# Performance work log

Measured on AMD Instinct MI355X. Metric: run time of the kernel, lower is better.

## Reference

```python
import jax, jax.numpy as jnp
import numpy as np

H = 512      # hidden_size
Z = 128      # z_dim
E = 512      # embedding_dim
D = 2 * H + Z  # GRU hidden / decoder state dim = 1152
V = 32000    # output_size
BS = 256
N = 128      # encoder nodes per source


def setup_inputs() -> dict:
    key = jax.random.key(0)
    ks = jax.random.split(key, 24)
    s = 0.05
    inp = {
        "prev_y": jax.random.normal(ks[0], (BS, E), jnp.float32),
        "prev_h": jax.random.normal(ks[1], (BS, D), jnp.float32),
        "equ_enc": jax.random.normal(ks[2], (BS, N, H), jnp.float32),
        "sns_enc": jax.random.normal(ks[3], (BS, N, H), jnp.float32),
        "z_sample": jax.random.normal(ks[4], (BS, Z), jnp.float32),
        "equ_mask": jax.random.randint(ks[5], (BS, N), 0, 2) > 0,
        "sns_mask": jax.random.randint(ks[6], (BS, N), 0, 2) > 0,
        # Attention (equ): W1: HxH, W2: HxD, vt: 1xH (torch Linear weight = [out,in])
        "W1e": jax.random.normal(ks[7], (H, H), jnp.float32) * s,
        "W2e": jax.random.normal(ks[8], (H, D), jnp.float32) * s,
        "vte": jax.random.normal(ks[9], (1, H), jnp.float32) * s,
        "W1s": jax.random.normal(ks[10], (H, H), jnp.float32) * s,
        "W2s": jax.random.normal(ks[11], (H, D), jnp.float32) * s,
        "vts": jax.random.normal(ks[12], (1, H), jnp.float32) * s,
        "plan_W": jax.random.normal(ks[13], (2, D), jnp.float32) * s,
        "plan_b": jax.random.normal(ks[14], (2,), jnp.float32) * s,
        "Wc": jax.random.normal(ks[15], (H, E + H), jnp.float32) * s,
        "bc": jax.random.normal(ks[16], (H,), jnp.float32) * s,
        # GRU: input H -> hidden D
        "w_ih": jax.random.normal(ks[17], (3 * D, H), jnp.float32) * s,
        "w_hh": jax.random.normal(ks[18], (3 * D, D), jnp.float32) * s,
        "b_ih": jax.random.normal(ks[19], (3 * D,), jnp.float32) * s,
        "b_hh": jax.random.normal(ks[20], (3 * D,), jnp.float32) * s,
        "Wout": jax.random.normal(ks[21], (V, D), jnp.float32) * s,
        "bout": jax.random.normal(ks[22], (V,), jnp.float32) * s,
    }
    return inp


def _attn(h, enc, mask, W1, W2, vt):
    # enc: (b,n,H), h: (b,D)
    et = jnp.einsum('bnh,kh->bnk', enc, W1)          # (b,n,H)
    dt = (h @ W2.T)[:, None, :]                       # (b,1,H)
    u = jnp.einsum('bnh,h->bn', jnp.tanh(et + dt), vt[0])
    u = jnp.where(mask, -jnp.inf, u)
    return jax.nn.softmax(u, axis=-1)                 # (b,n)


def reference(prev_y, prev_h, equ_enc, sns_enc, z_sample, equ_mask, sns_mask,
              W1e, W2e, vte, W1s, W2s, vts, plan_W, plan_b, Wc, bc,
              w_ih, w_hh, b_ih, b_hh, Wout, bout):
    aw_e = _attn(prev_h, equ_enc, equ_mask, W1e, W2e, vte)
    ctx_e = jnp.einsum('bn,bnh->bh', aw_e, equ_enc)
    aw_s = _attn(prev_h, sns_enc, sns_mask, W1s, W2s, vts)
    ctx_s = jnp.einsum('bn,bnh->bh', aw_s, sns_enc)
    plan = jax.nn.softmax(prev_h @ plan_W.T + plan_b, axis=-1)  # (b,2)
    combine = jnp.stack([ctx_e, ctx_s], axis=1)                  # (b,2,H)
    context = jnp.einsum('bk,bkh->bh', plan, combine)
    y_ctx = jnp.concatenate([prev_y, context], axis=-1)          # (b,E+H)
    x = y_ctx @ Wc.T + bc                                        # (b,H)
    # single-step GRU (torch gate order: r, z, n)
    gx = x @ w_ih.T + b_ih                                       # (b,3D)
    gh = prev_h @ w_hh.T + b_hh
    Dh = prev_h.shape[-1]
    gx_r, gx_z, gx_n = gx[:, :Dh], gx[:, Dh:2*Dh], gx[:, 2*Dh:]
    gh_r, gh_z, gh_n = gh[:, :Dh], gh[:, Dh:2*Dh], gh[:, 2*Dh:]
    r = jax.nn.sigmoid(gx_r + gh_r)
    zg = jax.nn.sigmoid(gx_z + gh_z)
    n = jnp.tanh(gx_n + r * gh_n)
    h_new = (1.0 - zg) * n + zg * prev_h                          # (b,D)
    dec_output = (h_new @ Wout.T + bout)[:, None, :]              # (b,1,V)
    dec_hidden = h_new[None]                                      # (1,b,D)
    return dec_output, dec_hidden, plan
```

## Files before the change

### kernel.cpp

```cpp
#include <hip/hip_runtime.h>
#include <stdint.h>
#include <math.h>

#define BS_  256
#define NSEQ 128
#define HH   512
#define DD   1152
#define VV   32000
#define BN_  (BS_*NSEQ)

typedef float  f32x4  __attribute__((ext_vector_type(4)));
typedef __bf16 bf16x8 __attribute__((ext_vector_type(8)));

__device__ __forceinline__ f32x4 mfma16(bf16x8 a, bf16x8 b, f32x4 c) {
    return __builtin_amdgcn_mfma_f32_16x16x32_bf16(a, b, c, 0, 0, 0);
}

__device__ __forceinline__ bf16x8 pack8(f32x4 a, f32x4 b) {
    bf16x8 v;
    v[0] = (__bf16)a[0]; v[1] = (__bf16)a[1]; v[2] = (__bf16)a[2]; v[3] = (__bf16)a[3];
    v[4] = (__bf16)b[0]; v[5] = (__bf16)b[1]; v[6] = (__bf16)b[2]; v[7] = (__bf16)b[3];
    return v;
}

__device__ __forceinline__ float tanh_fast(float x) {
    float e = __expf(2.f * x);
    return 1.f - __fdividef(2.f, e + 1.f);
}

__global__ __launch_bounds__(256) void k_tile128(
    const float* __restrict__ A, const float* __restrict__ B,
    const float* __restrict__ bias, float* __restrict__ C,
    int K, int ldc)
{
    const int rb = blockIdx.x * 128;
    const int cb = blockIdx.y * 128;
    const int t = threadIdx.x;
    const int w = t >> 6, wr = w >> 1, wc = w & 1;
    const int lane = t & 63, g = lane >> 4, r = lane & 15;
    const int s_row = t >> 1, s_h = t & 1;

    __shared__ bf16x8 sm[2][2][512];

    const float* Ap = A + (size_t)(rb + s_row) * K + s_h * 16;
    const float* Bp = B + (size_t)(cb + s_row) * K + s_h * 16;

    const int kg0 = 2 * s_h, kg1 = 2 * s_h + 1;
    const int swz0 = kg0 * 128 + ((s_row & 112) | ((s_row ^ (kg0 << 2)) & 15));
    const int swz1 = kg1 * 128 + ((s_row & 112) | ((s_row ^ (kg1 << 2)) & 15));

    int ai[4], bi[4];
    #pragma unroll
    for (int i = 0; i < 4; ++i) {
        ai[i] = g * 128 + wr * 64 + i * 16 + ((r ^ (g << 2)) & 15);
        bi[i] = g * 128 + wc * 64 + i * 16 + ((r ^ (g << 2)) & 15);
    }

    const int KS = K >> 5;
    f32x4 pa0 = ((const f32x4*)Ap)[0], pa1 = ((const f32x4*)Ap)[1],
          pa2 = ((const f32x4*)Ap)[2], pa3 = ((const f32x4*)Ap)[3];
    f32x4 pb0 = ((const f32x4*)Bp)[0], pb1 = ((const f32x4*)Bp)[1],
          pb2 = ((const f32x4*)Bp)[2], pb3 = ((const f32x4*)Bp)[3];

    f32x4 acc[4][4];
    #pragma unroll
    for (int i = 0; i < 4; ++i)
        #pragma unroll
        for (int j = 0; j < 4; ++j) acc[i][j] = (f32x4){0.f, 0.f, 0.f, 0.f};

    for (int kb = 0; kb < KS; ++kb) {
        const int buf = kb & 1;
        sm[buf][0][swz0] = pack8(pa0, pa1);
        sm[buf][0][swz1] = pack8(pa2, pa3);
        sm[buf][1][swz0] = pack8(pb0, pb1);
        sm[buf][1][swz1] = pack8(pb2, pb3);
        __syncthreads();
        if (kb + 1 < KS) {
            const float* a2 = Ap + (kb + 1) * 32;
            const float* b2 = Bp + (kb + 1) * 32;
            pa0 = ((const f32x4*)a2)[0]; pa1 = ((const f32x4*)a2)[1];
            pa2 = ((const f32x4*)a2)[2]; pa3 = ((const f32x4*)a2)[3];
            pb0 = ((const f32x4*)b2)[0]; pb1 = ((const f32x4*)b2)[1];
            pb2 = ((const f32x4*)b2)[2]; pb3 = ((const f32x4*)b2)[3];
        }
        bf16x8 af[4], bfr[4];
        #pragma unroll
        for (int i = 0; i < 4; ++i) af[i]  = sm[buf][0][ai[i]];
        #pragma unroll
        for (int j = 0; j < 4; ++j) bfr[j] = sm[buf][1][bi[j]];
        #pragma unroll
        for (int i = 0; i < 4; ++i)
            #pragma unroll
            for (int j = 0; j < 4; ++j)
                acc[i][j] = mfma16(af[i], bfr[j], acc[i][j]);
    }

    #pragma unroll
    for (int j = 0; j < 4; ++j) {
        const int col = cb + wc * 64 + j * 16 + r;
        const float bv = bias ? bias[col] : 0.f;
        #pragma unroll
        for (int i = 0; i < 4; ++i) {
            #pragma unroll
            for (int q = 0; q < 4; ++q) {
                const int row = rb + wr * 64 + i * 16 + g * 4 + q;
                C[(size_t)row * ldc + col] = acc[i][j][q] + bv;
            }
        }
    }
}

__global__ __launch_bounds__(256) void k_prevh(
    const float* __restrict__ prev_h, const float* __restrict__ W2e,
    const float* __restrict__ W2s, const float* __restrict__ w_hh,
    const float* __restrict__ b_hh,
    float* __restrict__ dt_e, float* __restrict__ dt_s, float* __restrict__ gh)
{
    const int cb = blockIdx.x * 64;
    const int rb = blockIdx.y * 64;
    const int t  = threadIdx.x;
    const int w = t >> 6, lane = t & 63, g = lane >> 4, r = lane & 15;
    const int s_row = t >> 2, s_kc = t & 3;
    const int K = DD;

    __shared__ bf16x8 sm[2][2][256];

    const float* Ap = prev_h + (size_t)(rb + s_row) * K + s_kc * 8;
    const float* Bp;
    {
        int brow = cb + s_row;
        if (cb < 512)        Bp = W2e + (size_t)brow * K;
        else if (cb < 1024)  Bp = W2s + (size_t)(brow - 512) * K;
        else                 Bp = w_hh + (size_t)(brow - 1024) * K;
        Bp += s_kc * 8;
    }

    const int KS = K >> 5;
    f32x4 pa0 = *(const f32x4*)Ap, pa1 = *(const f32x4*)(Ap + 4);
    f32x4 pb0 = *(const f32x4*)Bp, pb1 = *(const f32x4*)(Bp + 4);

    f32x4 acc[4] = {{0,0,0,0},{0,0,0,0},{0,0,0,0},{0,0,0,0}};

    for (int kb = 0; kb < KS; ++kb) {
        sm[kb & 1][0][s_kc * 64 + s_row] = pack8(pa0, pa1);
        sm[kb & 1][1][s_kc * 64 + s_row] = pack8(pb0, pb1);
        __syncthreads();
        if (kb + 1 < KS) {
            const float* a2 = Ap + (kb + 1) * 32;
            const float* b2 = Bp + (kb + 1) * 32;
            pa0 = *(const f32x4*)a2; pa1 = *(const f32x4*)(a2 + 4);
            pb0 = *(const f32x4*)b2; pb1 = *(const f32x4*)(b2 + 4);
        }
        bf16x8 af = sm[kb & 1][0][g * 64 + w * 16 + r];
        #pragma unroll
        for (int j = 0; j < 4; ++j) {
            bf16x8 bf = sm[kb & 1][1][g * 64 + j * 16 + r];
            acc[j] = mfma16(af, bf, acc[j]);
        }
    }

    #pragma unroll
    for (int j = 0; j < 4; ++j) {
        int col = cb + j * 16 + r;
        #pragma unroll
        for (int q = 0; q < 4; ++q) {
            int row = rb + w * 16 + g * 4 + q;
            float v = acc[j][q];
            if (cb < 512)       dt_e[(size_t)row * 512 + col] = v;
            else if (cb < 1024) dt_s[(size_t)row * 512 + (col - 512)] = v;
            else {
                int c0 = col - 1024;
                gh[(size_t)row * 3456 + c0] = v + b_hh[c0];
            }
        }
    }
}

__global__ __launch_bounds__(256) void k_attn(
    const float* __restrict__ enc_e, const float* __restrict__ enc_s,
    const float* __restrict__ W1e, const float* __restrict__ W1s,
    const float* __restrict__ vte, const float* __restrict__ vts,
    const float* __restrict__ dt_e, const float* __restrict__ dt_s,
    float* __restrict__ u)
{
    const int b = blockIdx.x;
    const int e = blockIdx.y;
    const float* enc = e ? enc_s : enc_e;
    const float* W1  = e ? W1s  : W1e;
    const float* vt  = e ? vts  : vte;
    const float* dt  = e ? dt_s : dt_e;

    __shared__ bf16x8 sm[2][2][512];
    __shared__ float uacc[128];

    const int t = threadIdx.x;
    const int w = t >> 6, wr = w >> 1, wc = w & 1;
    const int lane = t & 63, g = lane >> 4, r = lane & 15;
    const int s_row = t >> 1, s_h = t & 1;

    if (t < 128) uacc[t] = 0.f;

    const int kg0 = 2 * s_h, kg1 = 2 * s_h + 1;
    const int swz0 = kg0 * 128 + ((s_row & 112) | ((s_row ^ (kg0 << 2)) & 15));
    const int swz1 = kg1 * 128 + ((s_row & 112) | ((s_row ^ (kg1 << 2)) & 15));

    int ai[4], bi[4];
    #pragma unroll
    for (int i = 0; i < 4; ++i) {
        ai[i] = g * 128 + wr * 64 + i * 16 + ((r ^ (g << 2)) & 15);
        bi[i] = g * 128 + wc * 64 + i * 16 + ((r ^ (g << 2)) & 15);
    }

    const float* Abase = enc + (size_t)(b * 128 + s_row) * 512 + s_h * 16;

    f32x4 pa0, pa1, pa2, pa3, pb0, pb1, pb2, pb3;
    {
        const float* ap = Abase;
        const float* bp = W1 + (size_t)s_row * 512 + s_h * 16;
        pa0 = ((const f32x4*)ap)[0]; pa1 = ((const f32x4*)ap)[1];
        pa2 = ((const f32x4*)ap)[2]; pa3 = ((const f32x4*)ap)[3];
        pb0 = ((const f32x4*)bp)[0]; pb1 = ((const f32x4*)bp)[1];
        pb2 = ((const f32x4*)bp)[2]; pb3 = ((const f32x4*)bp)[3];
    }

    for (int nc = 0; nc < 4; ++nc) {
        f32x4 acc[4][4];
        #pragma unroll
        for (int i = 0; i < 4; ++i)
            #pragma unroll
            for (int j = 0; j < 4; ++j) acc[i][j] = (f32x4){0.f, 0.f, 0.f, 0.f};

        for (int kb = 0; kb < 16; ++kb) {
            const int buf = kb & 1;
            sm[buf][0][swz0] = pack8(pa0, pa1);
            sm[buf][0][swz1] = pack8(pa2, pa3);
            sm[buf][1][swz0] = pack8(pb0, pb1);
            sm[buf][1][swz1] = pack8(pb2, pb3);
            __syncthreads();

            int nnc = nc, nkb = kb + 1;
            if (nkb == 16) { nnc = nc + 1; nkb = 0; }
            if (nnc < 4) {
                const float* ap = Abase + nkb * 32;
                const float* bp = W1 + (size_t)(nnc * 128 + s_row) * 512 + nkb * 32 + s_h * 16;
                pa0 = ((const f32x4*)ap)[0]; pa1 = ((const f32x4*)ap)[1];
                pa2 = ((const f32x4*)ap)[2]; pa3 = ((const f32x4*)ap)[3];
                pb0 = ((const f32x4*)bp)[0]; pb1 = ((const f32x4*)bp)[1];
                pb2 = ((const f32x4*)bp)[2]; pb3 = ((const f32x4*)bp)[3];
            }

            bf16x8 af[4], bfr[4];
            #pragma unroll
            for (int i = 0; i < 4; ++i) af[i]  = sm[buf][0][ai[i]];
            #pragma unroll
            for (int j = 0; j < 4; ++j) bfr[j] = sm[buf][1][bi[j]];
            #pragma unroll
            for (int i = 0; i < 4; ++i)
                #pragma unroll
                for (int j = 0; j < 4; ++j)
                    acc[i][j] = mfma16(af[i], bfr[j], acc[i][j]);
        }

        float dv[4], vv[4];
        #pragma unroll
        for (int j = 0; j < 4; ++j) {
            int col = nc * 128 + wc * 64 + j * 16 + r;
            dv[j] = dt[(size_t)b * 512 + col];
            vv[j] = vt[col];
        }
        #pragma unroll
        for (int i = 0; i < 4; ++i) {
            #pragma unroll
            for (int q = 0; q < 4; ++q) {
                float s = 0.f;
                #pragma unroll
                for (int j = 0; j < 4; ++j)
                    s += vv[j] * tanh_fast(acc[i][j][q] + dv[j]);
                #pragma unroll
                for (int m = 1; m < 16; m <<= 1) s += __shfl_xor(s, m);
                if (r == 0) atomicAdd(&uacc[wr * 64 + i * 16 + g * 4 + q], s);
            }
        }
    }
    __syncthreads();
    if (t < 128) u[(size_t)e * BN_ + b * 128 + t] = uacc[t];
}

__global__ __launch_bounds__(256) void k_ctx(
    const float* __restrict__ u, const int* __restrict__ mask_e,
    const int* __restrict__ mask_s, const float* __restrict__ enc_e,
    const float* __restrict__ enc_s, const float* __restrict__ prev_h,
    const float* __restrict__ plan_W, const float* __restrict__ plan_b,
    const float* __restrict__ prev_y,
    float* __restrict__ y_ctx, float* __restrict__ plan_out)
{
    const int b = blockIdx.x;
    const int t = threadIdx.x;
    const int lane = t & 63, wid = t >> 6, half = t >> 7, n = t & 127;

    __shared__ float aw[2][128];
    __shared__ float red[16];
    __shared__ float planv[2];

    const int* mask = half ? mask_s : mask_e;
    float uv = u[(size_t)half * BN_ + b * 128 + n];
    bool msk = mask[b * 128 + n] != 0;
    float val = msk ? -3.4e38f : uv;

    float mx = val;
    #pragma unroll
    for (int m = 1; m < 64; m <<= 1) mx = fmaxf(mx, __shfl_xor(mx, m));
    if (lane == 0) red[wid] = mx;
    __syncthreads();
    mx = fmaxf(red[half * 2], red[half * 2 + 1]);
    float ex = msk ? 0.f : __expf(uv - mx);
    float sm = ex;
    #pragma unroll
    for (int m = 1; m < 64; m <<= 1) sm += __shfl_xor(sm, m);
    if (lane == 0) red[4 + wid] = sm;
    __syncthreads();
    sm = red[4 + half * 2] + red[4 + half * 2 + 1];
    aw[half][n] = ex / sm;

    float p0 = 0.f, p1 = 0.f;
    for (int i = t; i < DD; i += 256) {
        float hv = prev_h[(size_t)b * DD + i];
        p0 += hv * plan_W[i];
        p1 += hv * plan_W[DD + i];
    }
    #pragma unroll
    for (int m = 1; m < 64; m <<= 1) { p0 += __shfl_xor(p0, m); p1 += __shfl_xor(p1, m); }
    if (lane == 0) { red[8 + wid] = p0; red[12 + wid] = p1; }
    __syncthreads();
    if (t == 0) {
        float l0 = red[8] + red[9] + red[10] + red[11] + plan_b[0];
        float l1 = red[12] + red[13] + red[14] + red[15] + plan_b[1];
        float mm = fmaxf(l0, l1);
        float e0 = __expf(l0 - mm), e1 = __expf(l1 - mm);
        float ss = e0 + e1;
        planv[0] = e0 / ss; planv[1] = e1 / ss;
        plan_out[b * 2 + 0] = planv[0];
        plan_out[b * 2 + 1] = planv[1];
    }
    __syncthreads();

    float pl0 = planv[0], pl1 = planv[1];
    int col = blockIdx.y * 256 + t;
    float ae = 0.f, as2 = 0.f;
    const float* pe = enc_e + (size_t)b * 128 * 512 + col;
    const float* ps = enc_s + (size_t)b * 128 * 512 + col;
    #pragma unroll 8
    for (int nn = 0; nn < 128; ++nn) {
        ae  += aw[0][nn] * pe[(size_t)nn * 512];
        as2 += aw[1][nn] * ps[(size_t)nn * 512];
    }
    float ctx = pl0 * ae + pl1 * as2;
    y_ctx[(size_t)b * 1024 + col] = prev_y[(size_t)b * 512 + col];
    y_ctx[(size_t)b * 1024 + 512 + col] = ctx;
}

__global__ __launch_bounds__(256) void k_gemm_bias(
    const float* __restrict__ A, const float* __restrict__ B,
    const float* __restrict__ bias, float* __restrict__ C,
    int K, int ldc)
{
    const int cb = blockIdx.x * 64;
    const int rb = blockIdx.y * 64;
    const int t  = threadIdx.x;
    const int w = t >> 6, lane = t & 63, g = lane >> 4, r = lane & 15;
    const int s_row = t >> 2, s_kc = t & 3;

    __shared__ bf16x8 sm[2][2][256];

    const float* Ap = A + (size_t)(rb + s_row) * K + s_kc * 8;
    const float* Bp = B + (size_t)(cb + s_row) * K + s_kc * 8;

    const int KS = K >> 5;
    f32x4 pa0 = *(const f32x4*)Ap, pa1 = *(const f32x4*)(Ap + 4);
    f32x4 pb0 = *(const f32x4*)Bp, pb1 = *(const f32x4*)(Bp + 4);

    f32x4 acc[4] = {{0,0,0,0},{0,0,0,0},{0,0,0,0},{0,0,0,0}};

    for (int kb = 0; kb < KS; ++kb) {
        sm[kb & 1][0][s_kc * 64 + s_row] = pack8(pa0, pa1);
        sm[kb & 1][1][s_kc * 64 + s_row] = pack8(pb0, pb1);
        __syncthreads();
        if (kb + 1 < KS) {
            const float* a2 = Ap + (kb + 1) * 32;
            const float* b2 = Bp + (kb + 1) * 32;
            pa0 = *(const f32x4*)a2; pa1 = *(const f32x4*)(a2 + 4);
            pb0 = *(const f32x4*)b2; pb1 = *(const f32x4*)(b2 + 4);
        }
        bf16x8 af = sm[kb & 1][0][g * 64 + w * 16 + r];
        #pragma unroll
        for (int j = 0; j < 4; ++j) {
            bf16x8 bf = sm[kb & 1][1][g * 64 + j * 16 + r];
            acc[j] = mfma16(af, bf, acc[j]);
        }
    }
    #pragma unroll
    for (int j = 0; j < 4; ++j) {
        int col = cb + j * 16 + r;
        float bv = bias ? bias[col] : 0.f;
        #pragma unroll
        for (int q = 0; q < 4; ++q) {
            int row = rb + w * 16 + g * 4 + q;
            C[(size_t)row * ldc + col] = acc[j][q] + bv;
        }
    }
}

__global__ __launch_bounds__(384) void k_gru(
    const float* __restrict__ gx, const float* __restrict__ gh,
    const float* __restrict__ prev_h, float* __restrict__ h_new,
    float* __restrict__ out_hidden)
{
    int d = blockIdx.x * 384 + threadIdx.x;
    int b = blockIdx.y;
    size_t o3 = (size_t)b * 3456;
    float xr = gx[o3 + d], xz = gx[o3 + 1152 + d], xn = gx[o3 + 2304 + d];
    float hr = gh[o3 + d], hz = gh[o3 + 1152 + d], hn = gh[o3 + 2304 + d];
    float rr = 1.f / (1.f + __expf(-(xr + hr)));
    float zz = 1.f / (1.f + __expf(-(xz + hz)));
    float nv = tanhf(xn + rr * hn);
    float hv = (1.f - zz) * nv + zz * prev_h[(size_t)b * DD + d];
    h_new[(size_t)b * DD + d] = hv;
    out_hidden[(size_t)b * DD + d] = hv;
}

extern "C" void kernel_launch(void* const* d_in, const int* in_sizes, int n_in,
                              void* d_out, int out_size, void* d_ws, size_t ws_size,
                              hipStream_t stream)
{
    const float* prev_y = (const float*)d_in[0];
    const float* prev_h = (const float*)d_in[1];
    const float* enc_e  = (const float*)d_in[2];
    const float* enc_s  = (const float*)d_in[3];
    const int*   mask_e = (const int*)d_in[5];
    const int*   mask_s = (const int*)d_in[6];
    const float* W1e    = (const float*)d_in[7];
    const float* W2e    = (const float*)d_in[8];
    const float* vte    = (const float*)d_in[9];
    const float* W1s    = (const float*)d_in[10];
    const float* W2s    = (const float*)d_in[11];
    const float* vts    = (const float*)d_in[12];
    const float* plan_W = (const float*)d_in[13];
    const float* plan_b = (const float*)d_in[14];
    const float* Wc     = (const float*)d_in[15];
    const float* bc     = (const float*)d_in[16];
    const float* w_ih   = (const float*)d_in[17];
    const float* w_hh   = (const float*)d_in[18];
    const float* b_ih   = (const float*)d_in[19];
    const float* b_hh   = (const float*)d_in[20];
    const float* Wout   = (const float*)d_in[21];
    const float* bout   = (const float*)d_in[22];

    float* out = (float*)d_out;
    float* ws  = (float*)d_ws;
    float* dt_e  = ws;
    float* dt_s  = dt_e + 131072;
    float* gh    = dt_s + 131072;
    float* uu    = gh + 884736;
    float* y_ctx = uu + 65536;
    float* xx    = y_ctx + 262144;
    float* gx    = xx + 131072;
    float* h_new = gx + 884736;

    float* dec_out  = out;
    float* dec_hid  = out + 8192000;
    float* plan_out = out + 8486912;

    k_prevh<<<dim3(70, 4), 256, 0, stream>>>(prev_h, W2e, W2s, w_hh, b_hh,
                                             dt_e, dt_s, gh);

    k_attn<<<dim3(BS_, 2), 256, 0, stream>>>(
        enc_e, enc_s, W1e, W1s, vte, vts, dt_e, dt_s, uu);

    k_ctx<<<dim3(BS_, 2), 256, 0, stream>>>(uu, mask_e, mask_s, enc_e, enc_s,
                                            prev_h, plan_W, plan_b, prev_y,
                                            y_ctx, plan_out);

    k_gemm_bias<<<dim3(8, 4), 256, 0, stream>>>(y_ctx, Wc, bc, xx, 1024, 512);
    k_tile128<<<dim3(2, 27), 256, 0, stream>>>(xx, w_ih, b_ih, gx, 512, 3456);

    k_gru<<<dim3(3, BS_), 384, 0, stream>>>(gx, gh, prev_h, h_new, dec_hid);

    k_tile128<<<dim3(2, 250), 256, 0, stream>>>(h_new, Wout, bout, dec_out,
                                                1152, 32000);
}
```

Before: 575.0 us.

## Split attention over hidden chunks, vectorize context reduction, remap vocab GEMM blocks

The attention kernel is split into 2048 blocks, each covering one 128-column chunk of the hidden dimension, and writes partial scores that the context kernel sums. This raises parallelism and removes the serial chunk loop, at the cost of reloading the encoder tile four times. The context kernel now splits rows across two blocks, uses vectorized loads and combines results with global atomics into a zeroed buffer. The vocab projection gets its own kernel with a 1D grid whose remapping keeps both row tiles of the same Wout columns close together for L2 reuse. Workspace buffers are aliased to cut the footprint.

```diff
diff --git a/kernel.cpp b/kernel.cpp
--- a/kernel.cpp
+++ b/kernel.cpp
@@ -110,6 +110,93 @@
     }
 }
 
+__global__ __launch_bounds__(256) void k_vocab(
+    const float* __restrict__ A, const float* __restrict__ B,
+    const float* __restrict__ bias, float* __restrict__ C,
+    int K, int ldc)
+{
+    const int L = blockIdx.x;
+    const int p  = (L & 7) + ((L >> 4) << 3);
+    const int rr = (L >> 3) & 1;
+    if (p >= 250) return;
+    const int rb = rr * 128;
+    const int cb = p * 128;
+
+    const int t = threadIdx.x;
+    const int w = t >> 6, wr = w >> 1, wc = w & 1;
+    const int lane = t & 63, g = lane >> 4, r = lane & 15;
+    const int s_row = t >> 1, s_h = t & 1;
+
+    __shared__ bf16x8 sm[2][2][512];
+
+    const float* Ap = A + (size_t)(rb + s_row) * K + s_h * 16;
+    const float* Bp = B + (size_t)(cb + s_row) * K + s_h * 16;
+
+    const int kg0 = 2 * s_h, kg1 = 2 * s_h + 1;
+    const int swz0 = kg0 * 128 + ((s_row & 112) | ((s_row ^ (kg0 << 2)) & 15));
+    const int swz1 = kg1 * 128 + ((s_row & 112) | ((s_row ^ (kg1 << 2)) & 15));
+
+    int ai[4], bi[4];
+    #pragma unroll
+    for (int i = 0; i < 4; ++i) {
+        ai[i] = g * 128 + wr * 64 + i * 16 + ((r ^ (g << 2)) & 15);
+        bi[i] = g * 128 + wc * 64 + i * 16 + ((r ^ (g << 2)) & 15);
+    }
+
+    const int KS = K >> 5;
+    f32x4 pa0 = ((const f32x4*)Ap)[0], pa1 = ((const f32x4*)Ap)[1],
+          pa2 = ((const f32x4*)Ap)[2], pa3 = ((const f32x4*)Ap)[3];
+    f32x4 pb0 = ((const f32x4*)Bp)[0], pb1 = ((const f32x4*)Bp)[1],
+          pb2 = ((const f32x4*)Bp)[2], pb3 = ((const f32x4*)Bp)[3];
+
+    f32x4 acc[4][4];
+    #pragma unroll
+    for (int i = 0; i < 4; ++i)
+        #pragma unroll
+        for (int j = 0; j < 4; ++j) acc[i][j] = (f32x4){0.f, 0.f, 0.f, 0.f};
+
+    for (int kb = 0; kb < KS; ++kb) {
+        const int buf = kb & 1;
+        sm[buf][0][swz0] = pack8(pa0, pa1);
+        sm[buf][0][swz1] = pack8(pa2, pa3);
+        sm[buf][1][swz0] = pack8(pb0, pb1);
+        sm[buf][1][swz1] = pack8(pb2, pb3);
+        __syncthreads();
+        if (kb + 1 < KS) {
+            const float* a2 = Ap + (kb + 1) * 32;
+            const float* b2 = Bp + (kb + 1) * 32;
+            pa0 = ((const f32x4*)a2)[0]; pa1 = ((const f32x4*)a2)[1];
+            pa2 = ((const f32x4*)a2)[2]; pa3 = ((const f32x4*)a2)[3];
+            pb0 = ((const f32x4*)b2)[0]; pb1 = ((const f32x4*)b2)[1];
+            pb2 = ((const f32x4*)b2)[2]; pb3 = ((const f32x4*)b2)[3];
+        }
+        bf16x8 af[4], bfr[4];
+        #pragma unroll
+        for (int i = 0; i < 4; ++i) af[i]  = sm[buf][0][ai[i]];
+        #pragma unroll
+        for (int j = 0; j < 4; ++j) bfr[j] = sm[buf][1][bi[j]];
+        #pragma unroll
+        for (int i = 0; i < 4; ++i)
+            #pragma unroll
+            for (int j = 0; j < 4; ++j)
+                acc[i][j] = mfma16(af[i], bfr[j], acc[i][j]);
+    }
+
+    #pragma unroll
+    for (int j = 0; j < 4; ++j) {
+        const int col = cb + wc * 64 + j * 16 + r;
+        const float bv = bias[col];
+        #pragma unroll
+        for (int i = 0; i < 4; ++i) {
+            #pragma unroll
+            for (int q = 0; q < 4; ++q) {
+                const int row = rb + wr * 64 + i * 16 + g * 4 + q;
+                C[(size_t)row * ldc + col] = acc[i][j][q] + bv;
+            }
+        }
+    }
+}
+
 __global__ __launch_bounds__(256) void k_prevh(
     const float* __restrict__ prev_h, const float* __restrict__ W2e,
     const float* __restrict__ W2s, const float* __restrict__ w_hh,
@@ -181,25 +268,27 @@
     const float* __restrict__ W1e, const float* __restrict__ W1s,
     const float* __restrict__ vte, const float* __restrict__ vts,
     const float* __restrict__ dt_e, const float* __restrict__ dt_s,
-    float* __restrict__ u)
-{
-    const int b = blockIdx.x;
-    const int e = blockIdx.y;
+    float* __restrict__ u_part)
+{
+    const int L = blockIdx.x;
+    const int n = (L >> 3) & 3;
+    const int G = (L & 7) + ((L >> 5) << 3);
+    const int e = G >> 8;
+    const int b = G & 255;
+
     const float* enc = e ? enc_s : enc_e;
     const float* W1  = e ? W1s  : W1e;
     const float* vt  = e ? vts  : vte;
     const float* dt  = e ? dt_s : dt_e;
 
     __shared__ bf16x8 sm[2][2][512];
-    __shared__ float uacc[128];
+    __shared__ float upart[2][128];
 
     const int t = threadIdx.x;
     const int w = t >> 6, wr = w >> 1, wc = w & 1;
     const int lane = t & 63, g = lane >> 4, r = lane & 15;
     const int s_row = t >> 1, s_h = t & 1;
 
-    if (t < 128) uacc[t] = 0.f;
-
     const int kg0 = 2 * s_h, kg1 = 2 * s_h + 1;
     const int swz0 = kg0 * 128 + ((s_row & 112) | ((s_row ^ (kg0 << 2)) & 15));
     const int swz1 = kg1 * 128 + ((s_row & 112) | ((s_row ^ (kg1 << 2)) & 15));
@@ -211,83 +300,74 @@
         bi[i] = g * 128 + wc * 64 + i * 16 + ((r ^ (g << 2)) & 15);
     }
 
-    const float* Abase = enc + (size_t)(b * 128 + s_row) * 512 + s_h * 16;
-
-    f32x4 pa0, pa1, pa2, pa3, pb0, pb1, pb2, pb3;
-    {
-        const float* ap = Abase;
-        const float* bp = W1 + (size_t)s_row * 512 + s_h * 16;
-        pa0 = ((const f32x4*)ap)[0]; pa1 = ((const f32x4*)ap)[1];
-        pa2 = ((const f32x4*)ap)[2]; pa3 = ((const f32x4*)ap)[3];
-        pb0 = ((const f32x4*)bp)[0]; pb1 = ((const f32x4*)bp)[1];
-        pb2 = ((const f32x4*)bp)[2]; pb3 = ((const f32x4*)bp)[3];
-    }
-
-    for (int nc = 0; nc < 4; ++nc) {
-        f32x4 acc[4][4];
+    const float* Ap = enc + (size_t)(b * 128 + s_row) * 512 + s_h * 16;
+    const float* Bp = W1 + (size_t)(n * 128 + s_row) * 512 + s_h * 16;
+
+    f32x4 pa0 = ((const f32x4*)Ap)[0], pa1 = ((const f32x4*)Ap)[1],
+          pa2 = ((const f32x4*)Ap)[2], pa3 = ((const f32x4*)Ap)[3];
+    f32x4 pb0 = ((const f32x4*)Bp)[0], pb1 = ((const f32x4*)Bp)[1],
+          pb2 = ((const f32x4*)Bp)[2], pb3 = ((const f32x4*)Bp)[3];
+
+    f32x4 acc[4][4];
+    #pragma unroll
+    for (int i = 0; i < 4; ++i)
+        #pragma unroll
+        for (int j = 0; j < 4; ++j) acc[i][j] = (f32x4){0.f, 0.f, 0.f, 0.f};
+
+    for (int kb = 0; kb < 16; ++kb) {
+        const int buf = kb & 1;
+        sm[buf][0][swz0] = pack8(pa0, pa1);
+        sm[buf][0][swz1] = pack8(pa2, pa3);
+        sm[buf][1][swz0] = pack8(pb0, pb1);
+        sm[buf][1][swz1] = pack8(pb2, pb3);
+        __syncthreads();
+        if (kb + 1 < 16) {
+            const float* a2 = Ap + (kb + 1) * 32;
+            const float* b2 = Bp + (kb + 1) * 32;
+            pa0 = ((const f32x4*)a2)[0]; pa1 = ((const f32x4*)a2)[1];
+            pa2 = ((const f32x4*)a2)[2]; pa3 = ((const f32x4*)a2)[3];
+            pb0 = ((const f32x4*)b2)[0]; pb1 = ((const f32x4*)b2)[1];
+            pb2 = ((const f32x4*)b2)[2]; pb3 = ((const f32x4*)b2)[3];
+        }
+        bf16x8 af[4], bfr[4];
+        #pragma unroll
+        for (int i = 0; i < 4; ++i) af[i]  = sm[buf][0][ai[i]];
+        #pragma unroll
+        for (int j = 0; j < 4; ++j) bfr[j] = sm[buf][1][bi[j]];
         #pragma unroll
         for (int i = 0; i < 4; ++i)
             #pragma unroll
-            for (int j = 0; j < 4; ++j) acc[i][j] = (f32x4){0.f, 0.f, 0.f, 0.f};
-
-        for (int kb = 0; kb < 16; ++kb) {
-            const int buf = kb & 1;
-            sm[buf][0][swz0] = pack8(pa0, pa1);
-            sm[buf][0][swz1] = pack8(pa2, pa3);
-            sm[buf][1][swz0] = pack8(pb0, pb1);
-            sm[buf][1][swz1] = pack8(pb2, pb3);
-            __syncthreads();
-
-            int nnc = nc, nkb = kb + 1;
-            if (nkb == 16) { nnc = nc + 1; nkb = 0; }
-            if (nnc < 4) {
-                const float* ap = Abase + nkb * 32;
-                const float* bp = W1 + (size_t)(nnc * 128 + s_row) * 512 + nkb * 32 + s_h * 16;
-                pa0 = ((const f32x4*)ap)[0]; pa1 = ((const f32x4*)ap)[1];
-                pa2 = ((const f32x4*)ap)[2]; pa3 = ((const f32x4*)ap)[3];
-                pb0 = ((const f32x4*)bp)[0]; pb1 = ((const f32x4*)bp)[1];
-                pb2 = ((const f32x4*)bp)[2]; pb3 = ((const f32x4*)bp)[3];
-            }
-
-            bf16x8 af[4], bfr[4];
-            #pragma unroll
-            for (int i = 0; i < 4; ++i) af[i]  = sm[buf][0][ai[i]];
-            #pragma unroll
-            for (int j = 0; j < 4; ++j) bfr[j] = sm[buf][1][bi[j]];
-            #pragma unroll
-            for (int i = 0; i < 4; ++i)
-                #pragma unroll
-                for (int j = 0; j < 4; ++j)
-                    acc[i][j] = mfma16(af[i], bfr[j], acc[i][j]);
-        }
-
-        float dv[4], vv[4];
-        #pragma unroll
-        for (int j = 0; j < 4; ++j) {
-            int col = nc * 128 + wc * 64 + j * 16 + r;
-            dv[j] = dt[(size_t)b * 512 + col];
-            vv[j] = vt[col];
-        }
-        #pragma unroll
-        for (int i = 0; i < 4; ++i) {
-            #pragma unroll
-            for (int q = 0; q < 4; ++q) {
-                float s = 0.f;
-                #pragma unroll
-                for (int j = 0; j < 4; ++j)
-                    s += vv[j] * tanh_fast(acc[i][j][q] + dv[j]);
-                #pragma unroll
-                for (int m = 1; m < 16; m <<= 1) s += __shfl_xor(s, m);
-                if (r == 0) atomicAdd(&uacc[wr * 64 + i * 16 + g * 4 + q], s);
-            }
+            for (int j = 0; j < 4; ++j)
+                acc[i][j] = mfma16(af[i], bfr[j], acc[i][j]);
+    }
+
+    float dv[4], vv[4];
+    #pragma unroll
+    for (int j = 0; j < 4; ++j) {
+        int col = n * 128 + wc * 64 + j * 16 + r;
+        dv[j] = dt[(size_t)b * 512 + col];
+        vv[j] = vt[col];
+    }
+    #pragma unroll
+    for (int i = 0; i < 4; ++i) {
+        #pragma unroll
+        for (int q = 0; q < 4; ++q) {
+            float s = 0.f;
+            #pragma unroll
+            for (int j = 0; j < 4; ++j)
+                s += vv[j] * tanh_fast(acc[i][j][q] + dv[j]);
+            #pragma unroll
+            for (int m = 1; m < 16; m <<= 1) s += __shfl_xor(s, m);
+            if (r == 0) upart[wc][wr * 64 + i * 16 + g * 4 + q] = s;
         }
     }
     __syncthreads();
-    if (t < 128) u[(size_t)e * BN_ + b * 128 + t] = uacc[t];
+    if (t < 128)
+        u_part[((size_t)(n * 2 + e)) * BN_ + b * 128 + t] = upart[0][t] + upart[1][t];
 }
 
 __global__ __launch_bounds__(256) void k_ctx(
-    const float* __restrict__ u, const int* __restrict__ mask_e,
+    const float* __restrict__ u_part, const int* __restrict__ mask_e,
     const int* __restrict__ mask_s, const float* __restrict__ enc_e,
     const float* __restrict__ enc_s, const float* __restrict__ prev_h,
     const float* __restrict__ plan_W, const float* __restrict__ plan_b,
@@ -295,6 +375,7 @@
     float* __restrict__ y_ctx, float* __restrict__ plan_out)
 {
     const int b = blockIdx.x;
+    const int rh = blockIdx.y;
     const int t = threadIdx.x;
     const int lane = t & 63, wid = t >> 6, half = t >> 7, n = t & 127;
 
@@ -303,7 +384,10 @@
     __shared__ float planv[2];
 
     const int* mask = half ? mask_s : mask_e;
-    float uv = u[(size_t)half * BN_ + b * 128 + n];
+    float uv = u_part[(size_t)(0 * 2 + half) * BN_ + b * 128 + n]
+             + u_part[(size_t)(1 * 2 + half) * BN_ + b * 128 + n]
+             + u_part[(size_t)(2 * 2 + half) * BN_ + b * 128 + n]
+             + u_part[(size_t)(3 * 2 + half) * BN_ + b * 128 + n];
     bool msk = mask[b * 128 + n] != 0;
     float val = msk ? -3.4e38f : uv;
 
@@ -339,24 +423,34 @@
         float e0 = __expf(l0 - mm), e1 = __expf(l1 - mm);
         float ss = e0 + e1;
         planv[0] = e0 / ss; planv[1] = e1 / ss;
-        plan_out[b * 2 + 0] = planv[0];
-        plan_out[b * 2 + 1] = planv[1];
+        if (rh == 0) {
+            plan_out[b * 2 + 0] = planv[0];
+            plan_out[b * 2 + 1] = planv[1];
+        }
     }
     __syncthreads();
 
-    float pl0 = planv[0], pl1 = planv[1];
-    int col = blockIdx.y * 256 + t;
-    float ae = 0.f, as2 = 0.f;
-    const float* pe = enc_e + (size_t)b * 128 * 512 + col;
-    const float* ps = enc_s + (size_t)b * 128 * 512 + col;
-    #pragma unroll 8
-    for (int nn = 0; nn < 128; ++nn) {
-        ae  += aw[0][nn] * pe[(size_t)nn * 512];
-        as2 += aw[1][nn] * ps[(size_t)nn * 512];
-    }
-    float ctx = pl0 * ae + pl1 * as2;
-    y_ctx[(size_t)b * 1024 + col] = prev_y[(size_t)b * 512 + col];
-    y_ctx[(size_t)b * 1024 + 512 + col] = ctx;
+    const int ee = t >> 7;
+    const int tt = t & 127;
+    const float pl = planv[ee];
+    const float* base = (ee ? enc_s : enc_e) + (size_t)b * 65536 + (size_t)(rh * 64) * 512 + tt * 4;
+    f32x4 accv = {0.f, 0.f, 0.f, 0.f};
+    #pragma unroll 4
+    for (int row = 0; row < 64; ++row) {
+        f32x4 v = *(const f32x4*)(base + (size_t)row * 512);
+        float a = aw[ee][rh * 64 + row];
+        accv += a * v;
+    }
+    float* dst = y_ctx + (size_t)b * 1024 + 512 + tt * 4;
+    atomicAdd(dst + 0, pl * accv[0]);
+    atomicAdd(dst + 1, pl * accv[1]);
+    atomicAdd(dst + 2, pl * accv[2]);
+    atomicAdd(dst + 3, pl * accv[3]);
+
+    if (rh == 0 && t < 128) {
+        f32x4 v = *(const f32x4*)(prev_y + (size_t)b * 512 + t * 4);
+        *(f32x4*)(y_ctx + (size_t)b * 1024 + t * 4) = v;
+    }
 }
 
 __global__ __launch_bounds__(256) void k_gemm_bias(
@@ -457,26 +551,32 @@
 
     float* out = (float*)d_out;
     float* ws  = (float*)d_ws;
-    float* dt_e  = ws;
-    float* dt_s  = dt_e + 131072;
-    float* gh    = dt_s + 131072;
-    float* uu    = gh + 884736;
-    float* y_ctx = uu + 65536;
-    float* xx    = y_ctx + 262144;
-    float* gx    = xx + 131072;
-    float* h_new = gx + 884736;
+
+    float* gh     = ws;
+    float* big2   = ws + 884736;
+    float* upxx   = big2 + 884736;
+    float* y_ctx  = upxx + 262144;
+    float* h_new  = y_ctx + 262144;
+
+    float* dt_e  = big2;
+    float* dt_s  = big2 + 131072;
+    float* gx    = big2;
+    float* u_part = upxx;
+    float* xx    = upxx;
 
     float* dec_out  = out;
     float* dec_hid  = out + 8192000;
     float* plan_out = out + 8486912;
 
+    hipMemsetAsync(y_ctx, 0, 262144 * sizeof(float), stream);
+
     k_prevh<<<dim3(70, 4), 256, 0, stream>>>(prev_h, W2e, W2s, w_hh, b_hh,
                                              dt_e, dt_s, gh);
 
-    k_attn<<<dim3(BS_, 2), 256, 0, stream>>>(
-        enc_e, enc_s, W1e, W1s, vte, vts, dt_e, dt_s, uu);
-
-    k_ctx<<<dim3(BS_, 2), 256, 0, stream>>>(uu, mask_e, mask_s, enc_e, enc_s,
+    k_attn<<<dim3(2048), 256, 0, stream>>>(
+        enc_e, enc_s, W1e, W1s, vte, vts, dt_e, dt_s, u_part);
+
+    k_ctx<<<dim3(BS_, 2), 256, 0, stream>>>(u_part, mask_e, mask_s, enc_e, enc_s,
                                             prev_h, plan_W, plan_b, prev_y,
                                             y_ctx, plan_out);
 
@@ -485,6 +585,6 @@
 
     k_gru<<<dim3(3, BS_), 384, 0, stream>>>(gx, gh, prev_h, h_new, dec_hid);
 
-    k_tile128<<<dim3(2, 250), 256, 0, stream>>>(h_new, Wout, bout, dec_out,
-                                                1152, 32000);
-}
+    k_vocab<<<dim3(512), 256, 0, stream>>>(h_new, Wout, bout, dec_out,
+                                           1152, 32000);
+}
```

After: 554.6 us. -3.6%, faster.
